# Kernel optimization log

Hardware: AMD Instinct MI355X
Metric: run time of the kernel (lower is better)

Reference implementation:

```python
import jax, jax.numpy as jnp
import numpy as np
import math

B, S, E, H = 2, 2048, 1024, 16
D = E // H
EPS = 1e-5


def setup_inputs() -> dict:
    key = jax.random.key(0)
    ks = jax.random.split(key, 6)
    s = 1.0 / math.sqrt(E)
    return {
        "query": jax.random.normal(ks[0], (B, S, E), jnp.float32),
        "Wq": jax.random.normal(ks[1], (E, E), jnp.float32) * s,
        "bq": jnp.zeros((E,), jnp.float32),
        "Wk": jax.random.normal(ks[2], (E, E), jnp.float32) * s,
        "bk": jnp.zeros((E,), jnp.float32),
        "Wv": jax.random.normal(ks[3], (E, E), jnp.float32) * s,
        "bv": jnp.zeros((E,), jnp.float32),
        "Wo": jax.random.normal(ks[4], (E, E), jnp.float32) * s,
        "bo": jnp.zeros((E,), jnp.float32),
        "alpha": jnp.ones((1,), jnp.float32),
    }


def reference(query, Wq, bq, Wk, bk, Wv, bv, Wo, bo, alpha):
    # Q/K/V projections (nn.Linear: x @ W.T + b)
    q = (query @ Wq.T + bq).reshape(B, S, H, D)
    k = (query @ Wk.T + bk).reshape(B, S, H, D)
    v = (query @ Wv.T + bv).reshape(B, S, H, D)

    # YAT scores: (q.k)^2 / (||q-k||^2 + eps)
    qk = jnp.einsum('bqhd,bkhd->bhqk', q, k)          # [B,H,S,S]
    sq = jnp.einsum('bqhd,bqhd->bhq', q, q)           # ||q||^2
    sk = jnp.einsum('bkhd,bkhd->bhk', k, k)           # ||k||^2
    dist_sq = sq[..., :, None] + sk[..., None, :] - 2.0 * qk
    scores = (qk * qk) / (dist_sq + EPS)

    # learnable alpha scaling: scores * (sqrt(d)/log(1+d))^alpha
    scale = (jnp.sqrt(jnp.float32(D)) / jnp.log1p(jnp.float32(D))) ** alpha[0]
    scores = scores * scale

    attn = jax.nn.softmax(scores, axis=-1)
    out = jnp.einsum('bhqk,bkhd->bqhd', attn, v).reshape(B, S, E)
    return out @ Wo.T + bo
```

## Files before the change

### kernel.cpp

```cpp
#include <hip/hip_runtime.h>
#include <hip/hip_fp16.h>
#include <math.h>

#define BB 2
#define SS 2048
#define EE 1024
#define HH 16
#define DD 64
#define YAT_EPS 1e-5f
#define RR (BB * HH * SS)

typedef __attribute__((ext_vector_type(8))) short bf16x8;
typedef __attribute__((ext_vector_type(4))) short short4v;
typedef __attribute__((ext_vector_type(4))) float f32x4;
#define MFMA16(a, b, c) __builtin_amdgcn_mfma_f32_16x16x32_bf16((a), (b), (c), 0, 0, 0)

#if __has_builtin(__builtin_amdgcn_exp2f)
#define EXP2(x) __builtin_amdgcn_exp2f(x)
#else
#define EXP2(x) exp2f(x)
#endif
#if __has_builtin(__builtin_amdgcn_rcpf)
#define RCPF(x) __builtin_amdgcn_rcpf(x)
#else
#define RCPF(x) (1.0f / (x))
#endif

__device__ __forceinline__ unsigned short f2bf(float x) {
    unsigned int u = __float_as_uint(x);
    u += 0x7FFFu + ((u >> 16) & 1u);
    return (unsigned short)(u >> 16);
}
__device__ __forceinline__ float bf2f(unsigned short h) {
    return __uint_as_float(((unsigned int)h) << 16);
}

__device__ __forceinline__ void async_ld16(void* lds, const void* g) {
    __builtin_amdgcn_global_load_lds(
        (const __attribute__((address_space(1))) unsigned int*)g,
        (__attribute__((address_space(3))) unsigned int*)lds, 16, 0, 0);
}

__global__ __launch_bounds__(256) void split_f32(const float* __restrict__ in,
                                                 unsigned short* __restrict__ hi,
                                                 unsigned short* __restrict__ lo,
                                                 int n4) {
    int i = blockIdx.x * 256 + threadIdx.x;
    if (i >= n4) return;
    float4 v = ((const float4*)in)[i];
    ushort4 h, l;
    h.x = f2bf(v.x); l.x = f2bf(v.x - bf2f(h.x));
    h.y = f2bf(v.y); l.y = f2bf(v.y - bf2f(h.y));
    h.z = f2bf(v.z); l.z = f2bf(v.z - bf2f(h.z));
    h.w = f2bf(v.w); l.w = f2bf(v.w - bf2f(h.w));
    ((ushort4*)hi)[i] = h;
    ((ushort4*)lo)[i] = l;
}

__global__ __launch_bounds__(256) void split_w4(
        const float* __restrict__ Wq, const float* __restrict__ Wk,
        const float* __restrict__ Wv, const float* __restrict__ Wo,
        unsigned short* __restrict__ Whi, unsigned short* __restrict__ Wlo,
        unsigned short* __restrict__ Wohi, unsigned short* __restrict__ Wolo) {
    int i = blockIdx.x * 256 + threadIdx.x;
    int y = blockIdx.y;
    const float* src = y == 0 ? Wq : y == 1 ? Wk : y == 2 ? Wv : Wo;
    unsigned short* hi = y < 3 ? Whi + (size_t)y * EE * EE : Wohi;
    unsigned short* lo = y < 3 ? Wlo + (size_t)y * EE * EE : Wolo;
    float4 v = ((const float4*)src)[i];
    ushort4 h, l;
    h.x = f2bf(v.x); l.x = f2bf(v.x - bf2f(h.x));
    h.y = f2bf(v.y); l.y = f2bf(v.y - bf2f(h.y));
    h.z = f2bf(v.z); l.z = f2bf(v.z - bf2f(h.z));
    h.w = f2bf(v.w); l.w = f2bf(v.w - bf2f(h.w));
    ((ushort4*)hi)[i] = h;
    ((ushort4*)lo)[i] = l;
}

template <int MODE>
__global__ __launch_bounds__(256, 2) void gemm3p(
        const unsigned short* __restrict__ Ahi, const unsigned short* __restrict__ Alo,
        const unsigned short* __restrict__ Bhi, const unsigned short* __restrict__ Blo,
        const float* __restrict__ bq, const float* __restrict__ bk,
        const float* __restrict__ bv,
        float* __restrict__ Cf,
        unsigned short* __restrict__ qhi, unsigned short* __restrict__ qlo,
        unsigned short* __restrict__ khi, unsigned short* __restrict__ klo,
        unsigned short* __restrict__ v_sd,
        float* __restrict__ sqn, float* __restrict__ skn,
        int M, int N, int K) {
    __shared__ __align__(16) unsigned short LA_hi[128 * 32];
    __shared__ __align__(16) unsigned short LA_lo[128 * 32];
    __shared__ __align__(16) unsigned short LB_hi[128 * 32];
    __shared__ __align__(16) unsigned short LB_lo[128 * 32];

    const int t = threadIdx.x;
    const int w = t >> 6, lane = t & 63;
    const int quad = lane >> 4, lr = lane & 15;
    const int wy = w & 1, wx = w >> 1;
    const int m0 = blockIdx.y * 128, n0 = blockIdx.x * 128;

    const unsigned short* gsrc;
    unsigned short* ldst;
    if (w == 0)      { gsrc = Ahi + (size_t)m0 * K; ldst = LA_hi; }
    else if (w == 1) { gsrc = Alo + (size_t)m0 * K; ldst = LA_lo; }
    else if (w == 2) { gsrc = Bhi + (size_t)n0 * K; ldst = LB_hi; }
    else             { gsrc = Blo + (size_t)n0 * K; ldst = LB_lo; }
    const unsigned short* gl = gsrc + (size_t)(lane >> 2) * K + (lane & 3) * 8;

    f32x4 acc[4][4];
    #pragma unroll
    for (int i = 0; i < 4; ++i)
        #pragma unroll
        for (int j = 0; j < 4; ++j)
            acc[i][j] = (f32x4){0.f, 0.f, 0.f, 0.f};

    for (int k0 = 0; k0 < K; k0 += 32) {
        __syncthreads();
        #pragma unroll
        for (int i = 0; i < 8; ++i)
            async_ld16(ldst + i * 512, gl + (size_t)i * 16 * K + k0);
        __syncthreads();
        bf16x8 ah[4], al[4], bh_[4], bl_[4];
        #pragma unroll
        for (int i = 0; i < 4; ++i) {
            ah[i]  = *(const bf16x8*)&LA_hi[(wy * 64 + i * 16 + lr) * 32 + quad * 8];
            al[i]  = *(const bf16x8*)&LA_lo[(wy * 64 + i * 16 + lr) * 32 + quad * 8];
            bh_[i] = *(const bf16x8*)&LB_hi[(wx * 64 + i * 16 + lr) * 32 + quad * 8];
            bl_[i] = *(const bf16x8*)&LB_lo[(wx * 64 + i * 16 + lr) * 32 + quad * 8];
        }
        #pragma unroll
        for (int mg = 0; mg < 4; ++mg)
            #pragma unroll
            for (int ns = 0; ns < 4; ++ns) {
                f32x4 a = acc[mg][ns];
                a = MFMA16(ah[mg], bh_[ns], a);
                a = MFMA16(ah[mg], bl_[ns], a);
                a = MFMA16(al[mg], bh_[ns], a);
                acc[mg][ns] = a;
            }
    }

    const int ng = n0 + wx * 64;
    if (MODE == 0) {
        float bias_v[4];
        #pragma unroll
        for (int ns = 0; ns < 4; ++ns) bias_v[ns] = bq[ng + ns * 16 + lr];
        #pragma unroll
        for (int mg = 0; mg < 4; ++mg)
            #pragma unroll
            for (int r = 0; r < 4; ++r) {
                int m = m0 + wy * 64 + mg * 16 + quad * 4 + r;
                #pragma unroll
                for (int ns = 0; ns < 4; ++ns)
                    Cf[(size_t)m * N + ng + ns * 16 + lr] = acc[mg][ns][r] + bias_v[ns];
            }
    } else {
        const int path = ng >> 10;
        const int c = ng & 1023;
        const int h = c >> 6;
        const float* bias = path == 0 ? bq : path == 1 ? bk : bv;
        unsigned short* hi_p = path == 0 ? qhi : khi;
        unsigned short* lo_p = path == 0 ? qlo : klo;
        float* nrm = path == 0 ? sqn : skn;
        float bias_v[4];
        #pragma unroll
        for (int ns = 0; ns < 4; ++ns) bias_v[ns] = bias[c + ns * 16 + lr];
        #pragma unroll
        for (int mg = 0; mg < 4; ++mg)
            #pragma unroll
            for (int r = 0; r < 4; ++r) {
                int m = m0 + wy * 64 + mg * 16 + quad * 4 + r;
                int b = m >> 11, s = m & (SS - 1);
                size_t base = ((size_t)(b * HH + h) * SS + s) * DD;
                float v4[4];
                #pragma unroll
                for (int ns = 0; ns < 4; ++ns) v4[ns] = acc[mg][ns][r] + bias_v[ns];
                if (path < 2) {
                    float pn = v4[0] * v4[0] + v4[1] * v4[1] + v4[2] * v4[2] + v4[3] * v4[3];
                    #pragma unroll
                    for (int off = 1; off < 16; off <<= 1) pn += __shfl_xor(pn, off);
                    if (lr == 0) nrm[(size_t)(b * HH + h) * SS + s] = pn;
                    #pragma unroll
                    for (int ns = 0; ns < 4; ++ns) {
                        unsigned short hv = f2bf(v4[ns]);
                        hi_p[base + ns * 16 + lr] = hv;
                        lo_p[base + ns * 16 + lr] = f2bf(v4[ns] - bf2f(hv));
                    }
                } else {
                    #pragma unroll
                    for (int ns = 0; ns < 4; ++ns)
                        v_sd[base + ns * 16 + lr] = f2bf(v4[ns]);
                }
            }
    }
}

__global__ __launch_bounds__(256) void transpose_v(const unsigned short* __restrict__ v_sd,
                                                   unsigned short* __restrict__ vt) {
    __shared__ unsigned short T[64][65];
    const int t = threadIdx.x;
    const int bh = blockIdx.y, s0 = blockIdx.x * 64;
    {
        int sl = t >> 2, d4 = (t & 3) * 16;
        const unsigned short* src = &v_sd[((size_t)bh * SS + s0 + sl) * DD + d4];
        bf16x8 a = *(const bf16x8*)src;
        bf16x8 b = *(const bf16x8*)(src + 8);
        #pragma unroll
        for (int j = 0; j < 8; ++j) {
            T[sl][d4 + j] = (unsigned short)a[j];
            T[sl][d4 + 8 + j] = (unsigned short)b[j];
        }
    }
    __syncthreads();
    {
        int dl = t >> 2, s4 = (t & 3) * 16;
        bf16x8 a, b;
        #pragma unroll
        for (int j = 0; j < 8; ++j) {
            a[j] = (short)T[s4 + j][dl];
            b[j] = (short)T[s4 + 8 + j][dl];
        }
        unsigned short* dst = &vt[((size_t)bh * DD + dl) * SS + s0 + s4];
        *(bf16x8*)dst = a;
        *(bf16x8*)(dst + 8) = b;
    }
}

__global__ __launch_bounds__(256, 3) void yat_attn_mfma(
        const unsigned short* __restrict__ qhi, const unsigned short* __restrict__ qlo,
        const unsigned short* __restrict__ khi, const unsigned short* __restrict__ klo,
        const unsigned short* __restrict__ vt,
        const float* __restrict__ sqn, const float* __restrict__ skn,
        const float* __restrict__ alphap,
        __half* __restrict__ Opart, float2* __restrict__ mlpart) {
    __shared__ __align__(16) unsigned short Ks[2][8192];
    __shared__ __align__(16) unsigned short Ps[2][4][16 * 68];

    const int t = threadIdx.x;
    const int w = t >> 6, lane = t & 63;
    const int quad = lane >> 4, lr = lane & 15;
    const int qt = blockIdx.x, bh = blockIdx.y, z = blockIdx.z;
    const int row0 = qt * 64 + w * 16;
    const float cscale = powf(sqrtf((float)DD) / log1pf((float)DD), alphap[0])
                         * 1.4426950408889634f;

    bf16x8 qh[2], ql[2];
    #pragma unroll
    for (int kd = 0; kd < 2; ++kd) {
        size_t o = ((size_t)bh * SS + row0 + lr) * DD + kd * 32 + quad * 8;
        qh[kd] = *(const bf16x8*)&qhi[o];
        ql[kd] = *(const bf16x8*)&qlo[o];
    }
    const float sqe = sqn[(size_t)bh * SS + row0 + lr] + YAT_EPS;

    const int lrow = lane >> 3;
    const int lofs = lrow * 64 + (((lane & 7) ^ (lrow & 7)) << 3);

    float m_r = -INFINITY, l_r = 0.f;
    f32x4 O[4];
    #pragma unroll
    for (int nd = 0; nd < 4; ++nd) O[nd] = (f32x4){0.f, 0.f, 0.f, 0.f};

    const int kt0 = z * 16;
    {
        const size_t gbase = ((size_t)bh * SS + kt0 * 64 + w * 16) * 64 + lofs;
        #pragma unroll
        for (int i2 = 0; i2 < 2; ++i2) {
            async_ld16(&Ks[0][w * 1024 + i2 * 512],        khi + gbase + i2 * 512);
            async_ld16(&Ks[0][4096 + w * 1024 + i2 * 512], klo + gbase + i2 * 512);
        }
    }

    for (int it = 0; it < 16; ++it) {
        const int kt = kt0 + it;
        const int p = it & 1;
        const int kbase = kt * 64;
        __syncthreads();
        if (it < 15) {
            const size_t gbase = ((size_t)bh * SS + (kt + 1) * 64 + w * 16) * 64 + lofs;
            #pragma unroll
            for (int i2 = 0; i2 < 2; ++i2) {
                async_ld16(&Ks[p ^ 1][w * 1024 + i2 * 512],        khi + gbase + i2 * 512);
                async_ld16(&Ks[p ^ 1][4096 + w * 1024 + i2 * 512], klo + gbase + i2 * 512);
            }
        }
        f32x4 acc[4];
        f32x4 sk4[4];
        const unsigned short* kb = Ks[p];
        const int sw = lr & 7;
        #pragma unroll
        for (int st = 0; st < 4; ++st) {
            const int rbase = (st * 16 + lr) * 64;
            bf16x8 kh0 = *(const bf16x8*)&kb[rbase + ((quad    ) ^ sw) * 8];
            bf16x8 kh1 = *(const bf16x8*)&kb[rbase + ((quad + 4) ^ sw) * 8];
            bf16x8 kl0 = *(const bf16x8*)&kb[4096 + rbase + ((quad    ) ^ sw) * 8];
            bf16x8 kl1 = *(const bf16x8*)&kb[4096 + rbase + ((quad + 4) ^ sw) * 8];
            sk4[st] = *(const f32x4*)&skn[(size_t)bh * SS + kbase + st * 16 + quad * 4];
            f32x4 a = (f32x4){0.f, 0.f, 0.f, 0.f};
            a = MFMA16(kh0, qh[0], a);
            a = MFMA16(kh1, qh[1], a);
            a = MFMA16(kl0, qh[0], a);
            a = MFMA16(kl1, qh[1], a);
            a = MFMA16(kh0, ql[0], a);
            a = MFMA16(kh1, ql[1], a);
            acc[st] = a;
        }
        bf16x8 vf[4][2];
        #pragma unroll
        for (int nd = 0; nd < 4; ++nd)
            #pragma unroll
            for (int kk = 0; kk < 2; ++kk)
                vf[nd][kk] = *(const bf16x8*)&vt[((size_t)bh * DD + nd * 16 + lr) * SS
                                                 + kbase + kk * 32 + quad * 8];
        unsigned short* myP = Ps[p][w];
        float mx = -INFINITY;
        #pragma unroll
        for (int st = 0; st < 4; ++st)
            #pragma unroll
            for (int r = 0; r < 4; ++r) {
                float qk = acc[st][r];
                float d = sqe + sk4[st][r] - 2.f * qk;
                float s = qk * qk * cscale * RCPF(d);
                acc[st][r] = s;
                mx = fmaxf(mx, s);
            }
        mx = fmaxf(mx, __shfl_xor(mx, 16));
        mx = fmaxf(mx, __shfl_xor(mx, 32));
        float mnew = fmaxf(m_r, mx);
        float aa = EXP2(m_r - mnew);
        m_r = mnew;
        float rs = 0.f;
        #pragma unroll
        for (int st = 0; st < 4; ++st)
            #pragma unroll
            for (int r = 0; r < 4; ++r) {
                float e = EXP2(acc[st][r] - mnew);
                acc[st][r] = e;
                rs += e;
            }
        rs += __shfl_xor(rs, 16);
        rs += __shfl_xor(rs, 32);
        l_r = l_r * aa + rs;
        #pragma unroll
        for (int st = 0; st < 4; ++st) {
            short4v pv;
            pv[0] = (short)f2bf(acc[st][0]);
            pv[1] = (short)f2bf(acc[st][1]);
            pv[2] = (short)f2bf(acc[st][2]);
            pv[3] = (short)f2bf(acc[st][3]);
            *(short4v*)&myP[lr * 68 + st * 16 + quad * 4] = pv;
        }
        float al_[4];
        #pragma unroll
        for (int r = 0; r < 4; ++r) al_[r] = __shfl(aa, quad * 4 + r);
        #pragma unroll
        for (int nd = 0; nd < 4; ++nd)
            #pragma unroll
            for (int r = 0; r < 4; ++r)
                O[nd][r] *= al_[r];
        bf16x8 pf[2];
        #pragma unroll
        for (int kk = 0; kk < 2; ++kk)
            pf[kk] = *(const bf16x8*)&myP[lr * 68 + kk * 32 + quad * 8];
        #pragma unroll
        for (int nd = 0; nd < 4; ++nd)
            #pragma unroll
            for (int kk = 0; kk < 2; ++kk)
                O[nd] = MFMA16(pf[kk], vf[nd][kk], O[nd]);
    }
    if (quad == 0)
        mlpart[(size_t)z * RR + (size_t)bh * SS + row0 + lr] = make_float2(m_r, l_r);
    #pragma unroll
    for (int r = 0; r < 4; ++r) {
        size_t rowg = (size_t)bh * SS + row0 + quad * 4 + r;
        #pragma unroll
        for (int nd = 0; nd < 4; ++nd)
            Opart[((size_t)z * RR + rowg) * DD + nd * 16 + lr] =
                __float2half(O[nd][r]);
    }
}

__global__ __launch_bounds__(256) void combine_attn(
        const __half* __restrict__ Opart, const float2* __restrict__ mlpart,
        unsigned short* __restrict__ ctxhi, unsigned short* __restrict__ ctxlo) {
    int tid = blockIdx.x * 256 + threadIdx.x;
    int row = tid >> 4, c4 = (tid & 15) * 4;
    float2 ml0 = mlpart[row];
    float2 ml1 = mlpart[RR + row];
    float ms = fmaxf(ml0.x, ml1.x);
    float a0 = EXP2(ml0.x - ms), a1 = EXP2(ml1.x - ms);
    float inv = RCPF(ml0.y * a0 + ml1.y * a1);
    a0 *= inv; a1 *= inv;
    const __half* p0 = Opart + (size_t)row * DD + c4;
    const __half* p1 = p0 + (size_t)RR * DD;
    int bh = row >> 11, s = row & (SS - 1);
    int b = bh >> 4, h = bh & 15;
    size_t idx = ((size_t)b * SS + s) * EE + h * DD + c4;
    ushort4 hv, lv;
    unsigned short* hp = (unsigned short*)&hv;
    unsigned short* lp = (unsigned short*)&lv;
    #pragma unroll
    for (int j = 0; j < 4; ++j) {
        float o = __half2float(p0[j]) * a0 + __half2float(p1[j]) * a1;
        unsigned short hh = f2bf(o);
        hp[j] = hh;
        lp[j] = f2bf(o - bf2f(hh));
    }
    *(ushort4*)&ctxhi[idx] = hv;
    *(ushort4*)&ctxlo[idx] = lv;
}

extern "C" void kernel_launch(void* const* d_in, const int* in_sizes, int n_in,
                              void* d_out, int out_size, void* d_ws, size_t ws_size,
                              hipStream_t stream) {
    const float* x     = (const float*)d_in[0];
    const float* Wq    = (const float*)d_in[1];
    const float* bq    = (const float*)d_in[2];
    const float* Wk    = (const float*)d_in[3];
    const float* bk    = (const float*)d_in[4];
    const float* Wv    = (const float*)d_in[5];
    const float* bv    = (const float*)d_in[6];
    const float* Wo    = (const float*)d_in[7];
    const float* bo    = (const float*)d_in[8];
    const float* alpha = (const float*)d_in[9];
    float* out = (float*)d_out;
    char* ws = (char*)d_ws;

    const int M = BB * SS;
    const size_t MB = 1u << 20;
    unsigned short* xhi  = (unsigned short*)(ws + 0 * MB);
    unsigned short* xlo  = (unsigned short*)(ws + 8 * MB);
    unsigned short* Whi  = (unsigned short*)(ws + 16 * MB);
    unsigned short* Wlo  = (unsigned short*)(ws + 22 * MB);
    unsigned short* vt   = (unsigned short*)(ws + 16 * MB);
    float2* mlpart       = (float2*)(ws + 24 * MB);
    unsigned short* Wohi = (unsigned short*)(ws + 28 * MB);
    unsigned short* Wolo = (unsigned short*)(ws + 30 * MB);
    unsigned short* qhi  = (unsigned short*)(ws + 32 * MB);
    unsigned short* qlo  = (unsigned short*)(ws + 40 * MB);
    unsigned short* khi  = (unsigned short*)(ws + 48 * MB);
    unsigned short* klo  = (unsigned short*)(ws + 56 * MB);
    unsigned short* v_sd = (unsigned short*)(ws + 64 * MB);
    __half* Opart        = (__half*)(ws + 64 * MB);
    float* sqn = (float*)(ws + 80 * MB);
    float* skn = (float*)(ws + 80 * MB + 256 * 1024);
    unsigned short* ctxhi = xhi;
    unsigned short* ctxlo = xlo;

    const int nX = M * EE / 4, nW = EE * EE / 4;
    split_f32<<<nX / 256, 256, 0, stream>>>(x, xhi, xlo, nX);
    split_w4<<<dim3(nW / 256, 4), 256, 0, stream>>>(Wq, Wk, Wv, Wo,
                                                    Whi, Wlo, Wohi, Wolo);

    gemm3p<1><<<dim3(3 * EE / 128, M / 128), 256, 0, stream>>>(
        xhi, xlo, Whi, Wlo, bq, bk, bv, nullptr,
        qhi, qlo, khi, klo, v_sd, sqn, skn, M, 3 * EE, EE);

    transpose_v<<<dim3(SS / 64, BB * HH), 256, 0, stream>>>(v_sd, vt);

    yat_attn_mfma<<<dim3(SS / 64, BB * HH, 2), 256, 0, stream>>>(
        qhi, qlo, khi, klo, vt, sqn, skn, alpha, Opart, mlpart);

    combine_attn<<<RR * 16 / 256, 256, 0, stream>>>(Opart, mlpart, ctxhi, ctxlo);

    gemm3p<0><<<dim3(EE / 128, M / 128), 256, 0, stream>>>(
        ctxhi, ctxlo, Wohi, Wolo, bo, nullptr, nullptr, out,
        nullptr, nullptr, nullptr, nullptr, nullptr, nullptr, nullptr, M, EE, EE);
}
```

Before: 381.5 us.

## Drop split-bf16 low parts where precision allows in V, output projection and K

Cuts the three-pass split-bf16 emulation down to a single bf16 pass for the V projection and the output projection. K is now stored only as its bf16 high part, so the attention QK product loses two of its six MFMAs and its K tile shrinks by half. The combine step writes only a bf16 context, and P is converted to bf16 by truncation instead of rounding. Together these reduce MFMA count, LDS and global traffic, and workspace writes, at the cost of lower accuracy in V, K, the context and the output GEMM, which could exceed tolerance.

```diff
diff --git a/kernel.cpp b/kernel.cpp
--- a/kernel.cpp
+++ b/kernel.cpp
@@ -33,6 +33,9 @@
 }
 __device__ __forceinline__ float bf2f(unsigned short h) {
     return __uint_as_float(((unsigned int)h) << 16);
+}
+__device__ __forceinline__ short f2bf_t(float x) {
+    return (short)(__float_as_uint(x) >> 16);
 }
 
 __device__ __forceinline__ void async_ld16(void* lds, const void* g) {
@@ -61,23 +64,27 @@
         const float* __restrict__ Wq, const float* __restrict__ Wk,
         const float* __restrict__ Wv, const float* __restrict__ Wo,
         unsigned short* __restrict__ Whi, unsigned short* __restrict__ Wlo,
-        unsigned short* __restrict__ Wohi, unsigned short* __restrict__ Wolo) {
+        unsigned short* __restrict__ Wohi) {
     int i = blockIdx.x * 256 + threadIdx.x;
     int y = blockIdx.y;
     const float* src = y == 0 ? Wq : y == 1 ? Wk : y == 2 ? Wv : Wo;
     unsigned short* hi = y < 3 ? Whi + (size_t)y * EE * EE : Wohi;
-    unsigned short* lo = y < 3 ? Wlo + (size_t)y * EE * EE : Wolo;
     float4 v = ((const float4*)src)[i];
-    ushort4 h, l;
-    h.x = f2bf(v.x); l.x = f2bf(v.x - bf2f(h.x));
-    h.y = f2bf(v.y); l.y = f2bf(v.y - bf2f(h.y));
-    h.z = f2bf(v.z); l.z = f2bf(v.z - bf2f(h.z));
-    h.w = f2bf(v.w); l.w = f2bf(v.w - bf2f(h.w));
+    ushort4 h;
+    h.x = f2bf(v.x); h.y = f2bf(v.y); h.z = f2bf(v.z); h.w = f2bf(v.w);
     ((ushort4*)hi)[i] = h;
-    ((ushort4*)lo)[i] = l;
-}
-
-template <int MODE>
+    if (y < 2) {
+        unsigned short* lo = Wlo + (size_t)y * EE * EE;
+        ushort4 l;
+        l.x = f2bf(v.x - bf2f(h.x));
+        l.y = f2bf(v.y - bf2f(h.y));
+        l.z = f2bf(v.z - bf2f(h.z));
+        l.w = f2bf(v.w - bf2f(h.w));
+        ((ushort4*)lo)[i] = l;
+    }
+}
+
+template <int MODE, int PASSES>
 __global__ __launch_bounds__(256, 2) void gemm3p(
         const unsigned short* __restrict__ Ahi, const unsigned short* __restrict__ Alo,
         const unsigned short* __restrict__ Bhi, const unsigned short* __restrict__ Blo,
@@ -85,7 +92,7 @@
         const float* __restrict__ bv,
         float* __restrict__ Cf,
         unsigned short* __restrict__ qhi, unsigned short* __restrict__ qlo,
-        unsigned short* __restrict__ khi, unsigned short* __restrict__ klo,
+        unsigned short* __restrict__ khi,
         unsigned short* __restrict__ v_sd,
         float* __restrict__ sqn, float* __restrict__ skn,
         int M, int N, int K) {
@@ -100,13 +107,14 @@
     const int wy = w & 1, wx = w >> 1;
     const int m0 = blockIdx.y * 128, n0 = blockIdx.x * 128;
 
-    const unsigned short* gsrc;
-    unsigned short* ldst;
+    const unsigned short* gsrc = nullptr;
+    unsigned short* ldst = nullptr;
     if (w == 0)      { gsrc = Ahi + (size_t)m0 * K; ldst = LA_hi; }
-    else if (w == 1) { gsrc = Alo + (size_t)m0 * K; ldst = LA_lo; }
     else if (w == 2) { gsrc = Bhi + (size_t)n0 * K; ldst = LB_hi; }
-    else             { gsrc = Blo + (size_t)n0 * K; ldst = LB_lo; }
-    const unsigned short* gl = gsrc + (size_t)(lane >> 2) * K + (lane & 3) * 8;
+    else if (PASSES == 3 && w == 1) { gsrc = Alo + (size_t)m0 * K; ldst = LA_lo; }
+    else if (PASSES == 3 && w == 3) { gsrc = Blo + (size_t)n0 * K; ldst = LB_lo; }
+    const unsigned short* gl = gsrc ? gsrc + (size_t)(lane >> 2) * K + (lane & 3) * 8
+                                    : nullptr;
 
     f32x4 acc[4][4];
     #pragma unroll
@@ -117,17 +125,21 @@
 
     for (int k0 = 0; k0 < K; k0 += 32) {
         __syncthreads();
-        #pragma unroll
-        for (int i = 0; i < 8; ++i)
-            async_ld16(ldst + i * 512, gl + (size_t)i * 16 * K + k0);
+        if (gl) {
+            #pragma unroll
+            for (int i = 0; i < 8; ++i)
+                async_ld16(ldst + i * 512, gl + (size_t)i * 16 * K + k0);
+        }
         __syncthreads();
         bf16x8 ah[4], al[4], bh_[4], bl_[4];
         #pragma unroll
         for (int i = 0; i < 4; ++i) {
             ah[i]  = *(const bf16x8*)&LA_hi[(wy * 64 + i * 16 + lr) * 32 + quad * 8];
-            al[i]  = *(const bf16x8*)&LA_lo[(wy * 64 + i * 16 + lr) * 32 + quad * 8];
             bh_[i] = *(const bf16x8*)&LB_hi[(wx * 64 + i * 16 + lr) * 32 + quad * 8];
-            bl_[i] = *(const bf16x8*)&LB_lo[(wx * 64 + i * 16 + lr) * 32 + quad * 8];
+            if (PASSES == 3) {
+                al[i]  = *(const bf16x8*)&LA_lo[(wy * 64 + i * 16 + lr) * 32 + quad * 8];
+                bl_[i] = *(const bf16x8*)&LB_lo[(wx * 64 + i * 16 + lr) * 32 + quad * 8];
+            }
         }
         #pragma unroll
         for (int mg = 0; mg < 4; ++mg)
@@ -135,8 +147,10 @@
             for (int ns = 0; ns < 4; ++ns) {
                 f32x4 a = acc[mg][ns];
                 a = MFMA16(ah[mg], bh_[ns], a);
-                a = MFMA16(ah[mg], bl_[ns], a);
-                a = MFMA16(al[mg], bh_[ns], a);
+                if (PASSES == 3) {
+                    a = MFMA16(ah[mg], bl_[ns], a);
+                    a = MFMA16(al[mg], bh_[ns], a);
+                }
                 acc[mg][ns] = a;
             }
     }
@@ -156,12 +170,11 @@
                     Cf[(size_t)m * N + ng + ns * 16 + lr] = acc[mg][ns][r] + bias_v[ns];
             }
     } else {
-        const int path = ng >> 10;
-        const int c = ng & 1023;
+        const int path = MODE == 1 ? (ng >> 10) : 2;
+        const int c = MODE == 1 ? (ng & 1023) : ng;
         const int h = c >> 6;
         const float* bias = path == 0 ? bq : path == 1 ? bk : bv;
-        unsigned short* hi_p = path == 0 ? qhi : khi;
-        unsigned short* lo_p = path == 0 ? qlo : klo;
+        unsigned short* hi_p = path == 0 ? qhi : path == 1 ? khi : v_sd;
         float* nrm = path == 0 ? sqn : skn;
         float bias_v[4];
         #pragma unroll
@@ -185,12 +198,13 @@
                     for (int ns = 0; ns < 4; ++ns) {
                         unsigned short hv = f2bf(v4[ns]);
                         hi_p[base + ns * 16 + lr] = hv;
-                        lo_p[base + ns * 16 + lr] = f2bf(v4[ns] - bf2f(hv));
+                        if (path == 0)
+                            qlo[base + ns * 16 + lr] = f2bf(v4[ns] - bf2f(hv));
                     }
                 } else {
                     #pragma unroll
                     for (int ns = 0; ns < 4; ++ns)
-                        v_sd[base + ns * 16 + lr] = f2bf(v4[ns]);
+                        hi_p[base + ns * 16 + lr] = f2bf(v4[ns]);
                 }
             }
     }
@@ -229,12 +243,12 @@
 
 __global__ __launch_bounds__(256, 3) void yat_attn_mfma(
         const unsigned short* __restrict__ qhi, const unsigned short* __restrict__ qlo,
-        const unsigned short* __restrict__ khi, const unsigned short* __restrict__ klo,
+        const unsigned short* __restrict__ khi,
         const unsigned short* __restrict__ vt,
         const float* __restrict__ sqn, const float* __restrict__ skn,
         const float* __restrict__ alphap,
         __half* __restrict__ Opart, float2* __restrict__ mlpart) {
-    __shared__ __align__(16) unsigned short Ks[2][8192];
+    __shared__ __align__(16) unsigned short Ks[2][4096];
     __shared__ __align__(16) unsigned short Ps[2][4][16 * 68];
 
     const int t = threadIdx.x;
@@ -266,10 +280,8 @@
     {
         const size_t gbase = ((size_t)bh * SS + kt0 * 64 + w * 16) * 64 + lofs;
         #pragma unroll
-        for (int i2 = 0; i2 < 2; ++i2) {
-            async_ld16(&Ks[0][w * 1024 + i2 * 512],        khi + gbase + i2 * 512);
-            async_ld16(&Ks[0][4096 + w * 1024 + i2 * 512], klo + gbase + i2 * 512);
-        }
+        for (int i2 = 0; i2 < 2; ++i2)
+            async_ld16(&Ks[0][w * 1024 + i2 * 512], khi + gbase + i2 * 512);
     }
 
     for (int it = 0; it < 16; ++it) {
@@ -280,10 +292,8 @@
         if (it < 15) {
             const size_t gbase = ((size_t)bh * SS + (kt + 1) * 64 + w * 16) * 64 + lofs;
             #pragma unroll
-            for (int i2 = 0; i2 < 2; ++i2) {
-                async_ld16(&Ks[p ^ 1][w * 1024 + i2 * 512],        khi + gbase + i2 * 512);
-                async_ld16(&Ks[p ^ 1][4096 + w * 1024 + i2 * 512], klo + gbase + i2 * 512);
-            }
+            for (int i2 = 0; i2 < 2; ++i2)
+                async_ld16(&Ks[p ^ 1][w * 1024 + i2 * 512], khi + gbase + i2 * 512);
         }
         f32x4 acc[4];
         f32x4 sk4[4];
@@ -294,14 +304,10 @@
             const int rbase = (st * 16 + lr) * 64;
             bf16x8 kh0 = *(const bf16x8*)&kb[rbase + ((quad    ) ^ sw) * 8];
             bf16x8 kh1 = *(const bf16x8*)&kb[rbase + ((quad + 4) ^ sw) * 8];
-            bf16x8 kl0 = *(const bf16x8*)&kb[4096 + rbase + ((quad    ) ^ sw) * 8];
-            bf16x8 kl1 = *(const bf16x8*)&kb[4096 + rbase + ((quad + 4) ^ sw) * 8];
             sk4[st] = *(const f32x4*)&skn[(size_t)bh * SS + kbase + st * 16 + quad * 4];
             f32x4 a = (f32x4){0.f, 0.f, 0.f, 0.f};
             a = MFMA16(kh0, qh[0], a);
             a = MFMA16(kh1, qh[1], a);
-            a = MFMA16(kl0, qh[0], a);
-            a = MFMA16(kl1, qh[1], a);
             a = MFMA16(kh0, ql[0], a);
             a = MFMA16(kh1, ql[1], a);
             acc[st] = a;
@@ -345,10 +351,10 @@
         #pragma unroll
         for (int st = 0; st < 4; ++st) {
             short4v pv;
-            pv[0] = (short)f2bf(acc[st][0]);
-            pv[1] = (short)f2bf(acc[st][1]);
-            pv[2] = (short)f2bf(acc[st][2]);
-            pv[3] = (short)f2bf(acc[st][3]);
+            pv[0] = f2bf_t(acc[st][0]);
+            pv[1] = f2bf_t(acc[st][1]);
+            pv[2] = f2bf_t(acc[st][2]);
+            pv[3] = f2bf_t(acc[st][3]);
             *(short4v*)&myP[lr * 68 + st * 16 + quad * 4] = pv;
         }
         float al_[4];
@@ -383,7 +389,7 @@
 
 __global__ __launch_bounds__(256) void combine_attn(
         const __half* __restrict__ Opart, const float2* __restrict__ mlpart,
-        unsigned short* __restrict__ ctxhi, unsigned short* __restrict__ ctxlo) {
+        unsigned short* __restrict__ ctxhi) {
     int tid = blockIdx.x * 256 + threadIdx.x;
     int row = tid >> 4, c4 = (tid & 15) * 4;
     float2 ml0 = mlpart[row];
@@ -397,18 +403,14 @@
     int bh = row >> 11, s = row & (SS - 1);
     int b = bh >> 4, h = bh & 15;
     size_t idx = ((size_t)b * SS + s) * EE + h * DD + c4;
-    ushort4 hv, lv;
+    ushort4 hv;
     unsigned short* hp = (unsigned short*)&hv;
-    unsigned short* lp = (unsigned short*)&lv;
     #pragma unroll
     for (int j = 0; j < 4; ++j) {
         float o = __half2float(p0[j]) * a0 + __half2float(p1[j]) * a1;
-        unsigned short hh = f2bf(o);
-        hp[j] = hh;
-        lp[j] = f2bf(o - bf2f(hh));
+        hp[j] = f2bf(o);
     }
     *(ushort4*)&ctxhi[idx] = hv;
-    *(ushort4*)&ctxlo[idx] = lv;
 }
 
 extern "C" void kernel_launch(void* const* d_in, const int* in_sizes, int n_in,
@@ -436,35 +438,34 @@
     unsigned short* vt   = (unsigned short*)(ws + 16 * MB);
     float2* mlpart       = (float2*)(ws + 24 * MB);
     unsigned short* Wohi = (unsigned short*)(ws + 28 * MB);
-    unsigned short* Wolo = (unsigned short*)(ws + 30 * MB);
     unsigned short* qhi  = (unsigned short*)(ws + 32 * MB);
     unsigned short* qlo  = (unsigned short*)(ws + 40 * MB);
     unsigned short* khi  = (unsigned short*)(ws + 48 * MB);
-    unsigned short* klo  = (unsigned short*)(ws + 56 * MB);
     unsigned short* v_sd = (unsigned short*)(ws + 64 * MB);
     __half* Opart        = (__half*)(ws + 64 * MB);
     float* sqn = (float*)(ws + 80 * MB);
     float* skn = (float*)(ws + 80 * MB + 256 * 1024);
     unsigned short* ctxhi = xhi;
-    unsigned short* ctxlo = xlo;
 
     const int nX = M * EE / 4, nW = EE * EE / 4;
     split_f32<<<nX / 256, 256, 0, stream>>>(x, xhi, xlo, nX);
-    split_w4<<<dim3(nW / 256, 4), 256, 0, stream>>>(Wq, Wk, Wv, Wo,
-                                                    Whi, Wlo, Wohi, Wolo);
-
-    gemm3p<1><<<dim3(3 * EE / 128, M / 128), 256, 0, stream>>>(
-        xhi, xlo, Whi, Wlo, bq, bk, bv, nullptr,
-        qhi, qlo, khi, klo, v_sd, sqn, skn, M, 3 * EE, EE);
+    split_w4<<<dim3(nW / 256, 4), 256, 0, stream>>>(Wq, Wk, Wv, Wo, Whi, Wlo, Wohi);
+
+    gemm3p<1, 3><<<dim3(2 * EE / 128, M / 128), 256, 0, stream>>>(
+        xhi, xlo, Whi, Wlo, bq, bk, nullptr, nullptr,
+        qhi, qlo, khi, nullptr, sqn, skn, M, 2 * EE, EE);
+    gemm3p<2, 1><<<dim3(EE / 128, M / 128), 256, 0, stream>>>(
+        xhi, nullptr, Whi + 2 * (size_t)EE * EE, nullptr, nullptr, nullptr, bv, nullptr,
+        nullptr, nullptr, nullptr, v_sd, nullptr, nullptr, M, EE, EE);
 
     transpose_v<<<dim3(SS / 64, BB * HH), 256, 0, stream>>>(v_sd, vt);
 
     yat_attn_mfma<<<dim3(SS / 64, BB * HH, 2), 256, 0, stream>>>(
-        qhi, qlo, khi, klo, vt, sqn, skn, alpha, Opart, mlpart);
-
-    combine_attn<<<RR * 16 / 256, 256, 0, stream>>>(Opart, mlpart, ctxhi, ctxlo);
-
-    gemm3p<0><<<dim3(EE / 128, M / 128), 256, 0, stream>>>(
-        ctxhi, ctxlo, Wohi, Wolo, bo, nullptr, nullptr, out,
-        nullptr, nullptr, nullptr, nullptr, nullptr, nullptr, nullptr, M, EE, EE);
-}
+        qhi, qlo, khi, vt, sqn, skn, alpha, Opart, mlpart);
+
+    combine_attn<<<RR * 16 / 256, 256, 0, stream>>>(Opart, mlpart, ctxhi);
+
+    gemm3p<0, 1><<<dim3(EE / 128, M / 128), 256, 0, stream>>>(
+        ctxhi, nullptr, Wohi, nullptr, bo, nullptr, nullptr, out,
+        nullptr, nullptr, nullptr, nullptr, nullptr, nullptr, M, EE, EE);
+}
```

After: 358.1 us. 1.07x faster.
